# Kernel optimization log

Measured on AMD Instinct MI355X. Metric: run time of the kernel, lower is better.

## Reference

```python
import jax, jax.numpy as jnp
import numpy as np

B, C, L = 32, 512, 4096
H, K = 8, 3            # heads, kernel_size
D = C // H             # head dim
G = 32                 # GroupNorm groups
PAD = (K - 1) // 2
EPS = 1e-5
NEG = -1e30


def setup_inputs() -> dict:
    key = jax.random.key(0)
    ks = jax.random.split(key, 7)
    s = 0.02
    return {
        "x": jax.random.normal(ks[0], (B, C, L), dtype=jnp.float32),
        "gamma": jnp.ones((C,), dtype=jnp.float32),
        "beta": jnp.zeros((C,), dtype=jnp.float32),
        "W_k": jax.random.normal(ks[1], (C, H * D), dtype=jnp.float32) * s,
        "W_v": jax.random.normal(ks[2], (C, H * D), dtype=jnp.float32) * s,
        "W_o": jax.random.normal(ks[3], (H * D, C), dtype=jnp.float32) * s,
        "q": jax.random.normal(ks[4], (H, D), dtype=jnp.float32) * s,     # learned queries (QnA)
        "rpe": jax.random.normal(ks[5], (H, K), dtype=jnp.float32) * s,   # relative-position bias
    }


def _group_norm(x, gamma, beta):
    # x: (B, C, L); normalize over (C//G, L) within each of G groups
    b, c, l = x.shape
    xg = x.reshape(b, G, (c // G) * l)
    mu = jnp.mean(xg, axis=-1, keepdims=True)
    var = jnp.var(xg, axis=-1, keepdims=True)
    xn = ((xg - mu) * jax.lax.rsqrt(var + EPS)).reshape(b, c, l)
    return xn * gamma[None, :, None] + beta[None, :, None]


def reference(x, gamma, beta, W_k, W_v, W_o, q, rpe):
    h = _group_norm(x, gamma, beta)                     # (B, C, L)
    ht = jnp.transpose(h, (0, 2, 1))                    # (B, L, C)
    k = (ht @ W_k).reshape(B, L, H, D)                  # (B, L, H, D)
    v = (ht @ W_v).reshape(B, L, H, D)

    scale = 1.0 / np.sqrt(D).astype(np.float32)
    logits = jnp.einsum('blhd,hd->blh', k, q) * scale   # (B, L, H)

    # sliding windows of size K (zero-padded; -inf logits at boundaries)
    lp = jnp.pad(logits, ((0, 0), (PAD, PAD), (0, 0)), constant_values=NEG)
    lwin = jnp.stack([lp[:, j:j + L] for j in range(K)], axis=2)      # (B, L, K, H)
    lwin = lwin + jnp.transpose(rpe)[None, None]                       # rpe: (H,K)->(K,H)
    attn = jax.nn.softmax(lwin, axis=2)                                # (B, L, K, H)

    vp = jnp.pad(v, ((0, 0), (PAD, PAD), (0, 0), (0, 0)))
    vwin = jnp.stack([vp[:, j:j + L] for j in range(K)], axis=2)       # (B, L, K, H, D)
    o = jnp.einsum('blkh,blkhd->blhd', attn, vwin).reshape(B, L, H * D)

    out = (o @ W_o)                                      # (B, L, C)
    return x + jnp.transpose(out, (0, 2, 1))             # residual, (B, C, L)
```

## Files before the change

kernel.cpp:

```cpp
#include <hip/hip_runtime.h>

#define Bb 32
#define Cc 512
#define Ll 4096
#define Hh 8
#define Dd 64
#define Gg 32
#define BLt (Bb * Ll)
#define NKV 520
#define NKVPAD 640

typedef __attribute__((ext_vector_type(4))) float f32x4;
typedef __attribute__((ext_vector_type(8))) short short8;
typedef __attribute__((ext_vector_type(4))) short s16x4;
typedef __attribute__((ext_vector_type(4))) int int4v;

union U16 { int4v v; short s[8]; };

__device__ __forceinline__ float bf2f(short s) {
    unsigned u = ((unsigned)(unsigned short)s) << 16;
    float f; __builtin_memcpy(&f, &u, 4); return f;
}
__device__ __forceinline__ short f2bf(float f) {
    unsigned u; __builtin_memcpy(&u, &f, 4);
    u = (u + 0x7FFFu + ((u >> 16) & 1u)) >> 16;
    return (short)u;
}

__device__ __forceinline__ int kpack(int k) {
    int blk = k >> 5, r = k & 31;
    return blk * 32 + ((r & 15) >> 2) * 8 + ((r >> 4) << 2) + (r & 3);
}

__device__ __forceinline__ int swz_off(int row, int inner) {
    return row * 128 + (inner ^ ((row & 7) << 4));
}

__device__ __forceinline__ void gload16(const short* g, short* l) {
    __builtin_amdgcn_global_load_lds((const __attribute__((address_space(1))) unsigned int*)g,
                                     (__attribute__((address_space(3))) unsigned int*)l,
                                     16, 0, 0);
}

#define BAR() __builtin_amdgcn_s_barrier()
#define SFENCE() __builtin_amdgcn_sched_barrier(0)

__global__ void k_prep(const float* __restrict__ Wk, const float* __restrict__ Wv,
                       const float* __restrict__ Wo, const float* __restrict__ q,
                       short* __restrict__ Wct, short* __restrict__ Wot, int packWo)
{
    int bid = blockIdx.x, t = threadIdx.x;
    if (bid < NKVPAD) {
        int n = bid;
        if (n < 512) {
            for (int k = t; k < 512; k += 64)
                Wct[n * 512 + kpack(k)] = f2bf(Wv[k * 512 + n]);
        } else if (n < NKV) {
            int h = n - 512;
            for (int k = t; k < 512; k += 64) {
                float acc = 0.f;
                for (int d = 0; d < 64; ++d)
                    acc += Wk[k * 512 + h * 64 + d] * q[h * 64 + d];
                Wct[n * 512 + kpack(k)] = f2bf(acc * 0.125f);
            }
        } else {
            for (int k = t; k < 512; k += 64) Wct[n * 512 + kpack(k)] = 0;
        }
    } else {
        int c = bid - NKVPAD;
        for (int k = t; k < 512; k += 64)
            Wot[c * 512 + (packWo ? kpack(k) : k)] = f2bf(Wo[k * 512 + c]);
    }
}

__global__ void k_stats(const float* __restrict__ x, float* __restrict__ stats)
{
    int bg = blockIdx.x;
    const float* p = x + (size_t)bg * 65536;
    int t = threadIdx.x;
    float s = 0.f, ss = 0.f;
    for (int i = t * 4; i < 65536; i += 1024) {
        f32x4 v = *(const f32x4*)(p + i);
        s  += v[0] + v[1] + v[2] + v[3];
        ss += v[0]*v[0] + v[1]*v[1] + v[2]*v[2] + v[3]*v[3];
    }
    for (int o = 32; o > 0; o >>= 1) { s += __shfl_down(s, o); ss += __shfl_down(ss, o); }
    __shared__ float red[8];
    int lane = t & 63, w = t >> 6;
    if (lane == 0) { red[w] = s; red[4 + w] = ss; }
    __syncthreads();
    if (t == 0) {
        float S  = red[0] + red[1] + red[2] + red[3];
        float SS = red[4] + red[5] + red[6] + red[7];
        float mean = S * (1.0f / 65536.0f);
        float var  = SS * (1.0f / 65536.0f) - mean * mean;
        stats[bg * 2]     = mean;
        stats[bg * 2 + 1] = rsqrtf(var + 1e-5f);
    }
}

__global__ void k_norm_t(const float* __restrict__ x, const float* __restrict__ gamma,
                         const float* __restrict__ beta, const float* __restrict__ stats,
                         short* __restrict__ hT)
{
    __shared__ float tile[64 * 65];
    int b = blockIdx.z, c0 = blockIdx.y * 64, l0 = blockIdx.x * 64;
    int t = threadIdx.x;
    int lq = t & 15, cq = t >> 4;
    #pragma unroll
    for (int p = 0; p < 4; ++p) {
        int cl = cq + p * 16;
        int c = c0 + cl;
        float mean = stats[(b * 32 + (c >> 4)) * 2];
        float rstd = stats[(b * 32 + (c >> 4)) * 2 + 1];
        float a  = rstd * gamma[c];
        float bb = beta[c] - mean * a;
        f32x4 v = *(const f32x4*)(x + ((size_t)b << 21) + ((size_t)c << 12) + l0 + lq * 4);
        #pragma unroll
        for (int j = 0; j < 4; ++j) tile[cl * 65 + lq * 4 + j] = v[j] * a + bb;
    }
    __syncthreads();
    int ll = t >> 2, cq4 = t & 3;
    int bl = b * Ll + l0 + ll;
    short hbuf[16];
    #pragma unroll
    for (int j = 0; j < 16; ++j) hbuf[j] = f2bf(tile[(cq4 * 16 + j) * 65 + ll]);
    short* dst = hT + (size_t)bl * 512 + ((c0 >> 5) + (cq4 >> 1)) * 32 + ((cq4 & 1) << 2);
    #pragma unroll
    for (int jj = 0; jj < 4; ++jj) {
        s16x4 v4 = { hbuf[jj*4+0], hbuf[jj*4+1], hbuf[jj*4+2], hbuf[jj*4+3] };
        *(s16x4*)(dst + jj * 8) = v4;
    }
}


__launch_bounds__(256, 2)
__global__ void k_gemm1f(const short* __restrict__ A, const short* __restrict__ Bw,
                         short* __restrict__ vbuf, short* __restrict__ lbuf)
{
    __shared__ short sA[2][8192];
    __shared__ short sB[2][8192];
    __shared__ short wqlds[8192];
    const int t = threadIdx.x;
    const int nwg = 1024;
    const int bid = blockIdx.x;
    const int work = (bid & 7) * (nwg >> 3) + (bid >> 3);
    const int ntile = work & 3;
    const int n0 = ntile * 128;
    const int mbase = (work >> 2) * 512;

    const int lane = t & 63, wid = t >> 6;
    const int wm = wid >> 1, wn = wid & 1;
    const int g = lane >> 4, ln = lane & 15;

    {
        int row = t >> 5;
        int cp = (t & 31) * 2;
        int4v v0 = *(const int4v*)(Bw + (size_t)(512 + row) * 512 + cp * 8);
        int4v v1 = *(const int4v*)(Bw + (size_t)(512 + row) * 512 + cp * 8 + 8);
        *(int4v*)((char*)wqlds + row * 1024 + ((cp * 16) ^ ((row & 7) << 4))) = v0;
        *(int4v*)((char*)wqlds + row * 1024 + (((cp + 1) * 16) ^ ((row & 7) << 4))) = v1;
        int4v z = {0, 0, 0, 0};
        int row2 = 8 + (t >> 5);
        *(int4v*)((char*)wqlds + row2 * 1024 + ((cp * 16) ^ ((row2 & 7) << 4))) = z;
        *(int4v*)((char*)wqlds + row2 * 1024 + (((cp + 1) * 16) ^ ((row2 & 7) << 4))) = z;
    }
    asm volatile("s_waitcnt vmcnt(0) lgkmcnt(0)" ::: "memory");
    BAR(); SFENCE();

    const int srow = wid * 8 + (lane >> 3);
    const int sinner = (((lane & 7) ^ ((lane >> 3) & 7)) << 3);
    const short* gAs = A  + (size_t)(mbase + srow) * 512 + sinner;
    const short* gBs = Bw + (size_t)(n0 + srow) * 512 + sinner;

    f32x4 acc[4][4] = {};
    f32x4 accq[4] = {};

    auto stage = [&](int kt, int buf) {
        size_t offA = (size_t)(kt >> 3) * 65536 + (size_t)(kt & 7) * 64;
        size_t offB = (size_t)(kt & 7) * 64;
        #pragma unroll
        for (int gq = 0; gq < 4; ++gq) {
            gload16(gAs + (size_t)gq * 32 * 512 + offA, &sA[buf][gq * 2048 + wid * 512]);
            gload16(gBs + (size_t)gq * 32 * 512 + offB, &sB[buf][gq * 2048 + wid * 512]);
        }
    };
    auto compute = [&](int buf, int kk) {
        #pragma unroll
        for (int ks = 0; ks < 2; ++ks) {
            short8 af[4], bfr[4], bq;
            #pragma unroll
            for (int i = 0; i < 4; ++i) {
                af[i]  = *(const short8*)((const char*)&sA[buf][0] + swz_off(wm * 64 + i * 16 + ln, ks * 64 + g * 16));
                bfr[i] = *(const short8*)((const char*)&sB[buf][0] + swz_off(wn * 64 + i * 16 + ln, ks * 64 + g * 16));
            }
            bq = *(const short8*)((const char*)wqlds + ln * 1024 +
                                  ((kk * 128 + ks * 64 + g * 16) ^ ((ln & 7) << 4)));
            #pragma unroll
            for (int mi = 0; mi < 4; ++mi)
                #pragma unroll
                for (int ni = 0; ni < 4; ++ni)
                    acc[mi][ni] = __builtin_amdgcn_mfma_f32_16x16x32_bf16(af[mi], bfr[ni], acc[mi][ni], 0, 0, 0);
            #pragma unroll
            for (int mi = 0; mi < 4; ++mi)
                accq[mi] = __builtin_amdgcn_mfma_f32_16x16x32_bf16(af[mi], bq, accq[mi], 0, 0, 0);
        }
    };

    stage(0, 0); stage(1, 1);
    #pragma unroll 1
    for (int s = 0; s < 32; ++s) {
        if (s == 31)           asm volatile("s_waitcnt vmcnt(0)"  ::: "memory");
        else if ((s & 7) == 0 && s) asm volatile("s_waitcnt vmcnt(16)" ::: "memory");
        else                   asm volatile("s_waitcnt vmcnt(8)"  ::: "memory");
        BAR(); SFENCE();
        compute(s & 1, s & 7);
        SFENCE();
        if ((s & 7) == 7) {
            BAR();
            int m0 = mbase + (s >> 3) * 128;
            {
                short* scrW = &sB[s & 1][0] + wid * 2048;
                const int blkq = (lane & 7) >> 2, jq = lane & 3;
                #pragma unroll
                for (int p = 0; p < 2; ++p) {
                    #pragma unroll
                    for (int mh = 0; mh < 2; ++mh)
                        #pragma unroll
                        for (int ni = 0; ni < 4; ++ni)
                            #pragma unroll
                            for (int i = 0; i < 4; ++i)
                                scrW[(mh * 16 + g * 4 + i) * 64 + ni * 16 + ln] = f2bf(acc[p * 2 + mh][ni][i]);
                    asm volatile("s_waitcnt lgkmcnt(0)" ::: "memory"); SFENCE();
                    #pragma unroll
                    for (int it = 0; it < 4; ++it) {
                        int mrl = it * 8 + (lane >> 3);
                        const short* bp = scrW + mrl * 64 + blkq * 32;
                        s16x4 lo = *(const s16x4*)(bp + 4 * jq);
                        s16x4 hi = *(const s16x4*)(bp + 16 + 4 * jq);
                        union { int4v v; s16x4 h[2]; } ov;
                        ov.h[0] = lo; ov.h[1] = hi;
                        int m = m0 + wm * 64 + p * 32 + mrl;
                        int nc = n0 + wn * 64 + blkq * 32 + jq * 8;
                        *(int4v*)(vbuf + (size_t)m * 512 + nc) = ov.v;
                    }
                    asm volatile("s_waitcnt lgkmcnt(0)" ::: "memory"); SFENCE();
                }
            }
            if (ntile == 0 && wn == 0 && ln < 8) {
                #pragma unroll
                for (int mi = 0; mi < 4; ++mi)
                    #pragma unroll
                    for (int i = 0; i < 4; ++i) {
                        int m = m0 + wm * 64 + mi * 16 + g * 4 + i;
                        lbuf[(size_t)m * 8 + ln] = f2bf(accq[mi][i]);
                    }
            }
            #pragma unroll
            for (int mi = 0; mi < 4; ++mi) {
                #pragma unroll
                for (int ni = 0; ni < 4; ++ni)
                    acc[mi][ni] = (f32x4){0.f, 0.f, 0.f, 0.f};
                accq[mi] = (f32x4){0.f, 0.f, 0.f, 0.f};
            }
        }
        if (s < 30) { BAR(); stage(s + 2, s & 1); SFENCE(); }
    }
}

__global__ void k_combine(const short* __restrict__ vbuf, const short* __restrict__ lbuf,
                          const float* __restrict__ rpe, short* __restrict__ obuf)
{
    int t = threadIdx.x;
    int bl = blockIdx.x * 16 + (t >> 4);
    int blkd = t & 15;
    int h = blkd >> 1;
    int l = bl & (Ll - 1);
    int bm = (l == 0) ? bl : bl - 1;
    int bp = (l == Ll - 1) ? bl : bl + 1;
    float lg0 = (l > 0)      ? bf2f(lbuf[(size_t)bm * 8 + h]) + rpe[h * 3 + 0] : -1e30f;
    float lg1 =                bf2f(lbuf[(size_t)bl * 8 + h]) + rpe[h * 3 + 1];
    float lg2 = (l < Ll - 1) ? bf2f(lbuf[(size_t)bp * 8 + h]) + rpe[h * 3 + 2] : -1e30f;
    float m = fmaxf(lg1, fmaxf(lg0, lg2));
    float e0 = (l > 0)      ? __expf(lg0 - m) : 0.f;
    float e1 =                __expf(lg1 - m);
    float e2 = (l < Ll - 1) ? __expf(lg2 - m) : 0.f;
    float inv = 1.0f / (e0 + e1 + e2);
    float w0 = e0 * inv, w1 = e1 * inv, w2 = e2 * inv;

    const short8* vm = (const short8*)(vbuf + (size_t)bm * 512 + blkd * 32);
    const short8* v0 = (const short8*)(vbuf + (size_t)bl * 512 + blkd * 32);
    const short8* vp = (const short8*)(vbuf + (size_t)bp * 512 + blkd * 32);
    short8* dst = (short8*)(obuf + (size_t)bl * 512 + blkd * 32);
    #pragma unroll
    for (int qq = 0; qq < 4; ++qq) {
        short8 a = vm[qq], b = v0[qq], c = vp[qq], r;
        #pragma unroll
        for (int j = 0; j < 8; ++j)
            r[j] = f2bf(w0 * bf2f(a[j]) + w1 * bf2f(b[j]) + w2 * bf2f(c[j]));
        dst[qq] = r;
    }
}

__launch_bounds__(256, 2)
__global__ void k_gemm2f(const short* __restrict__ Wot, const short* __restrict__ obuf,
                         const float* __restrict__ x, float* __restrict__ out)
{
    __shared__ short sA[2][8192];
    __shared__ short sB[3][8192];
    const int t = threadIdx.x;
    const int nwg = 1024;
    const int bid = blockIdx.x;
    const int work = (bid & 7) * (nwg >> 3) + (bid >> 3);
    const int n0 = work * 128;

    const int lane = t & 63, wid = t >> 6;
    const int wm = wid >> 1, wn = wid & 1;
    const int g = lane >> 4, ln = lane & 15;

    const int srow = wid * 8 + (lane >> 3);
    const int sinner = (((lane & 7) ^ ((lane >> 3) & 7)) << 3);
    const short* gAs = Wot  + (size_t)srow * 512 + sinner;
    const short* gBs = obuf + (size_t)(n0 + srow) * 512 + sinner;

    const int r4 = lane >> 4, lcm = (lane & 15) * 4;
    const int ngE = n0 + wn * 64 + lcm;
    const size_t rowbase = ((size_t)(ngE >> 12) << 21) + (size_t)(ngE & (Ll - 1));
    const float* xrow = x + rowbase;
    float* outrow = out + rowbase;

    f32x4 acc[4][4] = {};
    f32x4 xp[4][4];

    auto stageA = [&](int s, int buf) {
        size_t off = (size_t)(s >> 3) * 65536 + (size_t)(s & 7) * 64;
        #pragma unroll
        for (int gq = 0; gq < 4; ++gq)
            gload16(gAs + (size_t)gq * 32 * 512 + off, &sA[buf][gq * 2048 + wid * 512]);
    };
    auto stageB = [&](int s, int buf) {
        size_t off = (size_t)(s & 7) * 64;
        #pragma unroll
        for (int gq = 0; gq < 4; ++gq)
            gload16(gBs + (size_t)gq * 32 * 512 + off, &sB[buf][gq * 2048 + wid * 512]);
    };
    auto xpf = [&](int tile) {
        int cb = tile * 128 + wm * 64;
        #pragma unroll
        for (int p = 0; p < 4; ++p)
            #pragma unroll
            for (int j = 0; j < 4; ++j)
                xp[p][j] = *(const f32x4*)(xrow + ((size_t)(cb + p * 16 + r4 + 4 * j) << 12));
    };
    auto compute = [&](int ab, int bb) {
        #pragma unroll
        for (int ks = 0; ks < 2; ++ks) {
            short8 af[4], bfr[4];
            #pragma unroll
            for (int i = 0; i < 4; ++i) {
                af[i]  = *(const short8*)((const char*)&sA[ab][0] + swz_off(wm * 64 + i * 16 + ln, ks * 64 + g * 16));
                bfr[i] = *(const short8*)((const char*)&sB[bb][0] + swz_off(wn * 64 + i * 16 + ln, ks * 64 + g * 16));
            }
            #pragma unroll
            for (int mi = 0; mi < 4; ++mi)
                #pragma unroll
                for (int ni = 0; ni < 4; ++ni)
                    acc[mi][ni] = __builtin_amdgcn_mfma_f32_16x16x32_bf16(af[mi], bfr[ni], acc[mi][ni], 0, 0, 0);
        }
    };

    stageA(0, 0); stageA(1, 1); stageB(0, 0); stageB(1, 1); stageB(2, 2);
    #pragma unroll 1
    for (int s = 0; s < 32; ++s) {
        if (s == 0)             asm volatile("s_waitcnt vmcnt(8)"  ::: "memory");
        else if (s == 31)       asm volatile("s_waitcnt vmcnt(0)"  ::: "memory");
        else if (s == 30)       asm volatile("s_waitcnt vmcnt(8)"  ::: "memory");
        else if ((s & 7) <= 2)  asm volatile("s_waitcnt vmcnt(28)" ::: "memory");
        else                    asm volatile("s_waitcnt vmcnt(12)" ::: "memory");
        BAR(); SFENCE();
        compute(s & 1, s % 3);
        SFENCE();
        if ((s & 7) == 7) {
            BAR();
            float* scr = (float*)((char*)&sA[s & 1][0] + wid * 4096);
            int m0c = (s >> 3) * 128;
            #pragma unroll
            for (int p = 0; p < 4; ++p) {
                #pragma unroll
                for (int ni = 0; ni < 4; ++ni)
                    #pragma unroll
                    for (int i = 0; i < 4; ++i) {
                        int r = g * 4 + i;
                        int col = (ni * 16 + ln) ^ ((((r & 3) ^ (r >> 2)) & 3) << 4);
                        scr[r * 64 + col] = acc[p][ni][i];
                    }
                asm volatile("s_waitcnt lgkmcnt(0)" ::: "memory"); SFENCE();
                #pragma unroll
                for (int j = 0; j < 4; ++j) {
                    int rr = r4 + 4 * j;
                    int cst = lcm ^ ((((rr & 3) ^ (rr >> 2)) & 3) << 4);
                    f32x4 sv = *(const f32x4*)&scr[rr * 64 + cst];
                    int c = m0c + wm * 64 + p * 16 + rr;
                    *(f32x4*)(outrow + ((size_t)c << 12)) = xp[p][j] + sv;
                }
                asm volatile("s_waitcnt lgkmcnt(0)" ::: "memory"); SFENCE();
            }
            #pragma unroll
            for (int mi = 0; mi < 4; ++mi)
                #pragma unroll
                for (int ni = 0; ni < 4; ++ni)
                    acc[mi][ni] = (f32x4){0.f, 0.f, 0.f, 0.f};
        }
        if (s < 30) {
            BAR();
            stageA(s + 2, s & 1);
            if (s < 29) stageB(s + 3, (s + 3) % 3);
            if ((s & 7) == 0) xpf(s >> 3);
            SFENCE();
        }
    }
}

__launch_bounds__(256, 2)
__global__ void k_gemm1_fb(const short* __restrict__ A, const short* __restrict__ Bw,
                           short* __restrict__ kv)
{
    __shared__ short sA[2][8192];
    __shared__ short sB[2][8192];
    const int t = threadIdx.x;
    const int m0 = blockIdx.y * 128;
    const int n0 = blockIdx.x * 128;
    const int lane = t & 63, wid = t >> 6;
    const int wm = wid >> 1, wn = wid & 1;
    const int g = lane >> 4, ln = lane & 15;

    const int srow = wid * 8 + (lane >> 3);
    const int sinner = (((lane & 7) ^ ((lane >> 3) & 7)) << 3);
    const short* gAs = A  + (size_t)(m0 + srow) * 512 + sinner;
    const short* gBs = Bw + (size_t)(n0 + srow) * 512 + sinner;

    f32x4 acc[4][4] = {};

    auto stage = [&](int kt, int buf) {
        #pragma unroll
        for (int gq = 0; gq < 4; ++gq) {
            gload16(gAs + (size_t)gq * 32 * 512 + kt * 64, &sA[buf][gq * 2048 + wid * 512]);
            gload16(gBs + (size_t)gq * 32 * 512 + kt * 64, &sB[buf][gq * 2048 + wid * 512]);
        }
    };
    auto compute = [&](int buf) {
        #pragma unroll
        for (int ks = 0; ks < 2; ++ks) {
            short8 af[4], bfr[4];
            #pragma unroll
            for (int i = 0; i < 4; ++i) {
                af[i]  = *(const short8*)((const char*)&sA[buf][0] + swz_off(wm * 64 + i * 16 + ln, ks * 64 + g * 16));
                bfr[i] = *(const short8*)((const char*)&sB[buf][0] + swz_off(wn * 64 + i * 16 + ln, ks * 64 + g * 16));
            }
            #pragma unroll
            for (int mi = 0; mi < 4; ++mi)
                #pragma unroll
                for (int ni = 0; ni < 4; ++ni)
                    acc[mi][ni] = __builtin_amdgcn_mfma_f32_16x16x32_bf16(af[mi], bfr[ni], acc[mi][ni], 0, 0, 0);
        }
    };

    stage(0, 0);
    __syncthreads();
    #pragma unroll 1
    for (int kt = 0; kt < 8; ++kt) {
        if (kt < 7) stage(kt + 1, (kt + 1) & 1);
        compute(kt & 1);
        __syncthreads();
    }

    #pragma unroll
    for (int mi = 0; mi < 4; ++mi)
        #pragma unroll
        for (int ni = 0; ni < 4; ++ni) {
            int n = n0 + wn * 64 + ni * 16 + ln;
            if (n < NKV) {
                #pragma unroll
                for (int i = 0; i < 4; ++i) {
                    int m = m0 + wm * 64 + mi * 16 + g * 4 + i;
                    kv[(size_t)m * NKV + n] = f2bf(acc[mi][ni][i]);
                }
            }
        }
}

__global__ void k_attnw(const short* __restrict__ kv, const float* __restrict__ rpe,
                        float* __restrict__ attnW)
{
    int tid = blockIdx.x * 256 + threadIdx.x;
    int bl = tid >> 3, h = tid & 7;
    int l = bl & (Ll - 1);
    float lg[3];
    #pragma unroll
    for (int j = 0; j < 3; ++j) {
        bool valid = (j == 1) || (j == 0 && l > 0) || (j == 2 && l < Ll - 1);
        lg[j] = valid ? (bf2f(kv[(size_t)(bl + j - 1) * NKV + 512 + h]) + rpe[h * 3 + j])
                      : -1e30f;
    }
    float m = fmaxf(lg[0], fmaxf(lg[1], lg[2]));
    float e0 = __expf(lg[0] - m), e1 = __expf(lg[1] - m), e2 = __expf(lg[2] - m);
    float inv = 1.0f / (e0 + e1 + e2);
    f32x4 w = { e0 * inv, e1 * inv, e2 * inv, 0.0f };
    *(f32x4*)(attnW + (size_t)bl * 32 + h * 4) = w;
}

__launch_bounds__(256, 2)
__global__ void k_gemm2_fused(const short* __restrict__ Wot, const short* __restrict__ kv,
                              const float* __restrict__ attnW, const float* __restrict__ x,
                              float* __restrict__ out)
{
    __shared__ short sA[2][8192];
    __shared__ short sB[2][8192];
    const int t = threadIdx.x;
    const int m0 = blockIdx.x * 128;
    const int n0 = blockIdx.y * 128;
    const int lane = t & 63, wid = t >> 6;
    const int wm = wid >> 1, wn = wid & 1;
    const int g = lane >> 4, ln = lane & 15;
    const int sr = t >> 1, ksh = t & 1;

    const short* gA = Wot + (size_t)(m0 + sr) * 512 + ksh * 32;
    const int nrow = n0 + sr;
    const int lpos = nrow & (Ll - 1);
    const int nm1 = (lpos == 0) ? nrow : nrow - 1;
    const int np1 = (lpos == Ll - 1) ? nrow : nrow + 1;
    const short* gV0 = kv + (size_t)nrow * NKV + ksh * 32;
    const short* gVm = kv + (size_t)nm1  * NKV + ksh * 32;
    const short* gVp = kv + (size_t)np1  * NKV + ksh * 32;
    const float* gW = attnW + (size_t)nrow * 32;

    f32x4 acc[4][4] = {};
    U16 ra[4], rbm[4], rb0[4], rbp[4];
    f32x4 wv;

    auto load_tile = [&](int kt) {
        #pragma unroll
        for (int qq = 0; qq < 4; ++qq) {
            ra[qq].v  = *(const int4v*)(gA  + kt * 64 + qq * 8);
            rbm[qq].v = *(const int4v*)(gVm + kt * 64 + qq * 8);
            rb0[qq].v = *(const int4v*)(gV0 + kt * 64 + qq * 8);
            rbp[qq].v = *(const int4v*)(gVp + kt * 64 + qq * 8);
        }
        wv = *(const f32x4*)(gW + kt * 4);
    };
    auto write_tile = [&](int buf) {
        short ob[32];
        #pragma unroll
        for (int qq = 0; qq < 4; ++qq)
            #pragma unroll
            for (int j = 0; j < 8; ++j) {
                float o = wv[0] * bf2f(rbm[qq].s[j]) + wv[1] * bf2f(rb0[qq].s[j])
                        + wv[2] * bf2f(rbp[qq].s[j]);
                ob[qq * 8 + j] = f2bf(o);
            }
        #pragma unroll
        for (int f = 0; f < 4; ++f) {
            U16 wa, wb;
            #pragma unroll
            for (int j = 0; j < 4; ++j) {
                wa.s[j]     = ra[f >> 1].s[(f & 1) * 4 + j];
                wa.s[4 + j] = ra[2 + (f >> 1)].s[(f & 1) * 4 + j];
                wb.s[j]     = ob[4 * f + j];
                wb.s[4 + j] = ob[16 + 4 * f + j];
            }
            int off = swz_off(sr, ksh * 64 + f * 16);
            *(int4v*)((char*)&sA[buf][0] + off) = wa.v;
            *(int4v*)((char*)&sB[buf][0] + off) = wb.v;
        }
    };
    auto compute = [&](int buf) {
        #pragma unroll
        for (int ks = 0; ks < 2; ++ks) {
            short8 af[4], bfr[4];
            #pragma unroll
            for (int i = 0; i < 4; ++i) {
                af[i]  = *(const short8*)((const char*)&sA[buf][0] + swz_off(wm * 64 + i * 16 + ln, ks * 64 + g * 16));
                bfr[i] = *(const short8*)((const char*)&sB[buf][0] + swz_off(wn * 64 + i * 16 + ln, ks * 64 + g * 16));
            }
            #pragma unroll
            for (int mi = 0; mi < 4; ++mi)
                #pragma unroll
                for (int ni = 0; ni < 4; ++ni)
                    acc[mi][ni] = __builtin_amdgcn_mfma_f32_16x16x32_bf16(af[mi], bfr[ni], acc[mi][ni], 0, 0, 0);
        }
    };

    load_tile(0); write_tile(0); __syncthreads();
    #pragma unroll 1
    for (int kt = 0; kt < 8; ++kt) {
        if (kt < 7) load_tile(kt + 1);
        compute(kt & 1);
        if (kt < 7) write_tile((kt + 1) & 1);
        __syncthreads();
    }

    #pragma unroll
    for (int mi = 0; mi < 4; ++mi)
        #pragma unroll
        for (int ni = 0; ni < 4; ++ni)
            #pragma unroll
            for (int i = 0; i < 4; ++i) {
                int c = m0 + wm * 64 + mi * 16 + g * 4 + i;
                int ng = n0 + wn * 64 + ni * 16 + ln;
                int b = ng >> 12, l = ng & (Ll - 1);
                size_t off = ((size_t)b << 21) | ((size_t)c << 12) | (size_t)l;
                out[off] = x[off] + acc[mi][ni][i];
            }
}

extern "C" void kernel_launch(void* const* d_in, const int* in_sizes, int n_in,
                              void* d_out, int out_size, void* d_ws, size_t ws_size,
                              hipStream_t stream)
{
    const float* x     = (const float*)d_in[0];
    const float* gamma = (const float*)d_in[1];
    const float* beta  = (const float*)d_in[2];
    const float* Wk    = (const float*)d_in[3];
    const float* Wv    = (const float*)d_in[4];
    const float* Wo    = (const float*)d_in[5];
    const float* q     = (const float*)d_in[6];
    const float* rpe   = (const float*)d_in[7];
    float* out = (float*)d_out;
    char* ws = (char*)d_ws;

    const size_t MB128 = 134217728ull;
    const size_t MAIN_WS = MB128 * 2 + 655360 + 524288 + 2097152 + 8192;

    if (ws_size >= MAIN_WS) {
        short* obuf  = (short*)(ws);
        short* vbuf  = (short*)(ws + MB128);
        short* Wct   = (short*)(ws + 2 * MB128);
        short* Wot   = (short*)(ws + 2 * MB128 + 655360);
        short* lbuf  = (short*)(ws + 2 * MB128 + 655360 + 524288);
        float* stats = (float*)(ws + 2 * MB128 + 655360 + 524288 + 2097152);
        short* hT    = (short*)d_out;

        k_prep<<<1152, 64, 0, stream>>>(Wk, Wv, Wo, q, Wct, Wot, 1);
        k_stats<<<1024, 256, 0, stream>>>(x, stats);
        k_norm_t<<<dim3(64, 8, 32), 256, 0, stream>>>(x, gamma, beta, stats, hT);
        k_gemm1f<<<1024, 256, 0, stream>>>(hT, Wct, vbuf, lbuf);
        k_combine<<<8192, 256, 0, stream>>>(vbuf, lbuf, rpe, obuf);
        k_gemm2f<<<1024, 256, 0, stream>>>(Wot, obuf, x, out);
    } else {
        short* Wct   = (short*)(ws + 0);
        short* Wot   = (short*)(ws + 655360);
        float* stats = (float*)(ws + 1179648);
        float* attnW = (float*)(ws + 1187840);
        short* kv    = (short*)(ws + 17965056);
        short* hT    = (short*)d_out;

        k_prep<<<1152, 64, 0, stream>>>(Wk, Wv, Wo, q, Wct, Wot, 0);
        k_stats<<<1024, 256, 0, stream>>>(x, stats);
        k_norm_t<<<dim3(64, 8, 32), 256, 0, stream>>>(x, gamma, beta, stats, hT);
        k_gemm1_fb<<<dim3(5, 1024), 256, 0, stream>>>(hT, Wct, kv);
        k_attnw<<<4096, 256, 0, stream>>>(kv, rpe, attnW);
        k_gemm2_fused<<<dim3(4, 1024), 256, 0, stream>>>(Wot, kv, attnW, x, out);
    }
}
```

Baseline: 545.6 us.

## Fuse windowed attention combine into output GEMM B-operand staging

Replaces the separate combine kernel, which wrote a full bf16 obuf, with a small kernel that writes only per-position softmax weights. The output GEMM now loads the three neighbouring V rows into registers, mixes them with the weights from LDS, and writes the combined bf16 tile into LDS as its B operand. This removes one full write and re-read of a 128 MB intermediate. In exchange, V reads in the GEMM triple, the pipeline becomes synchronous with vmcnt(0) waits every step, and the x prefetch becomes an inline load in the epilogue.

```diff
diff --git a/kernel.cpp b/kernel.cpp
--- a/kernel.cpp
+++ b/kernel.cpp
@@ -37,6 +37,11 @@
 }
 
 __device__ __forceinline__ void gload16(const short* g, short* l) {
+    __builtin_amdgcn_global_load_lds((const __attribute__((address_space(1))) unsigned int*)g,
+                                     (__attribute__((address_space(3))) unsigned int*)l,
+                                     16, 0, 0);
+}
+__device__ __forceinline__ void gload16f(const float* g, float* l) {
     __builtin_amdgcn_global_load_lds((const __attribute__((address_space(1))) unsigned int*)g,
                                      (__attribute__((address_space(3))) unsigned int*)l,
                                      16, 0, 0);
@@ -132,7 +137,6 @@
         *(s16x4*)(dst + jj * 8) = v4;
     }
 }
-
 
 __launch_bounds__(256, 2)
 __global__ void k_gemm1f(const short* __restrict__ A, const short* __restrict__ Bw,
@@ -268,46 +272,32 @@
     }
 }
 
-__global__ void k_combine(const short* __restrict__ vbuf, const short* __restrict__ lbuf,
-                          const float* __restrict__ rpe, short* __restrict__ obuf)
-{
-    int t = threadIdx.x;
-    int bl = blockIdx.x * 16 + (t >> 4);
-    int blkd = t & 15;
-    int h = blkd >> 1;
+__global__ void k_attnw2(const short* __restrict__ lbuf, const float* __restrict__ rpe,
+                         float* __restrict__ attnW)
+{
+    int tid = blockIdx.x * 256 + threadIdx.x;
+    int bl = tid >> 3, h = tid & 7;
     int l = bl & (Ll - 1);
-    int bm = (l == 0) ? bl : bl - 1;
-    int bp = (l == Ll - 1) ? bl : bl + 1;
-    float lg0 = (l > 0)      ? bf2f(lbuf[(size_t)bm * 8 + h]) + rpe[h * 3 + 0] : -1e30f;
-    float lg1 =                bf2f(lbuf[(size_t)bl * 8 + h]) + rpe[h * 3 + 1];
-    float lg2 = (l < Ll - 1) ? bf2f(lbuf[(size_t)bp * 8 + h]) + rpe[h * 3 + 2] : -1e30f;
+    float lg0 = (l > 0)      ? bf2f(lbuf[(size_t)(bl - 1) * 8 + h]) + rpe[h * 3 + 0] : -1e30f;
+    float lg1 =                bf2f(lbuf[(size_t)bl * 8 + h])       + rpe[h * 3 + 1];
+    float lg2 = (l < Ll - 1) ? bf2f(lbuf[(size_t)(bl + 1) * 8 + h]) + rpe[h * 3 + 2] : -1e30f;
     float m = fmaxf(lg1, fmaxf(lg0, lg2));
     float e0 = (l > 0)      ? __expf(lg0 - m) : 0.f;
     float e1 =                __expf(lg1 - m);
     float e2 = (l < Ll - 1) ? __expf(lg2 - m) : 0.f;
     float inv = 1.0f / (e0 + e1 + e2);
-    float w0 = e0 * inv, w1 = e1 * inv, w2 = e2 * inv;
-
-    const short8* vm = (const short8*)(vbuf + (size_t)bm * 512 + blkd * 32);
-    const short8* v0 = (const short8*)(vbuf + (size_t)bl * 512 + blkd * 32);
-    const short8* vp = (const short8*)(vbuf + (size_t)bp * 512 + blkd * 32);
-    short8* dst = (short8*)(obuf + (size_t)bl * 512 + blkd * 32);
-    #pragma unroll
-    for (int qq = 0; qq < 4; ++qq) {
-        short8 a = vm[qq], b = v0[qq], c = vp[qq], r;
-        #pragma unroll
-        for (int j = 0; j < 8; ++j)
-            r[j] = f2bf(w0 * bf2f(a[j]) + w1 * bf2f(b[j]) + w2 * bf2f(c[j]));
-        dst[qq] = r;
-    }
+    f32x4 w = { e0 * inv, e1 * inv, e2 * inv, 0.0f };
+    *(f32x4*)(attnW + (size_t)bl * 32 + h * 4) = w;
 }
 
 __launch_bounds__(256, 2)
-__global__ void k_gemm2f(const short* __restrict__ Wot, const short* __restrict__ obuf,
-                         const float* __restrict__ x, float* __restrict__ out)
+__global__ void k_gemm2f(const short* __restrict__ Wot, const short* __restrict__ vbuf,
+                         const float* __restrict__ attnW, const float* __restrict__ x,
+                         float* __restrict__ out)
 {
     __shared__ short sA[2][8192];
-    __shared__ short sB[3][8192];
+    __shared__ short sBc[2][8192];
+    __shared__ float wlds[4096];
     const int t = threadIdx.x;
     const int nwg = 1024;
     const int bid = blockIdx.x;
@@ -320,8 +310,19 @@
 
     const int srow = wid * 8 + (lane >> 3);
     const int sinner = (((lane & 7) ^ ((lane >> 3) & 7)) << 3);
-    const short* gAs = Wot  + (size_t)srow * 512 + sinner;
-    const short* gBs = obuf + (size_t)(n0 + srow) * 512 + sinner;
+    const short* gAs = Wot + (size_t)srow * 512 + sinner;
+
+    const short* gV0[4]; const short* gVm[4]; const short* gVp[4];
+    #pragma unroll
+    for (int q2 = 0; q2 < 4; ++q2) {
+        int r = n0 + srow + 32 * q2;
+        int l = r & (Ll - 1);
+        int rm = (l == 0) ? r : r - 1;
+        int rp = (l == Ll - 1) ? r : r + 1;
+        gV0[q2] = vbuf + (size_t)r  * 512 + sinner;
+        gVm[q2] = vbuf + (size_t)rm * 512 + sinner;
+        gVp[q2] = vbuf + (size_t)rp * 512 + sinner;
+    }
 
     const int r4 = lane >> 4, lcm = (lane & 15) * 4;
     const int ngE = n0 + wn * 64 + lcm;
@@ -330,7 +331,7 @@
     float* outrow = out + rowbase;
 
     f32x4 acc[4][4] = {};
-    f32x4 xp[4][4];
+    U16 Rm[4], R0[4], Rp[4];
 
     auto stageA = [&](int s, int buf) {
         size_t off = (size_t)(s >> 3) * 65536 + (size_t)(s & 7) * 64;
@@ -338,28 +339,39 @@
         for (int gq = 0; gq < 4; ++gq)
             gload16(gAs + (size_t)gq * 32 * 512 + off, &sA[buf][gq * 2048 + wid * 512]);
     };
-    auto stageB = [&](int s, int buf) {
-        size_t off = (size_t)(s & 7) * 64;
-        #pragma unroll
-        for (int gq = 0; gq < 4; ++gq)
-            gload16(gBs + (size_t)gq * 32 * 512 + off, &sB[buf][gq * 2048 + wid * 512]);
-    };
-    auto xpf = [&](int tile) {
-        int cb = tile * 128 + wm * 64;
-        #pragma unroll
-        for (int p = 0; p < 4; ++p)
-            #pragma unroll
-            for (int j = 0; j < 4; ++j)
-                xp[p][j] = *(const f32x4*)(xrow + ((size_t)(cb + p * 16 + r4 + 4 * j) << 12));
-    };
-    auto compute = [&](int ab, int bb) {
+    auto loadR = [&](int s1) {
+        size_t off = (size_t)(s1 & 7) * 64;
+        #pragma unroll
+        for (int q2 = 0; q2 < 4; ++q2) {
+            Rm[q2].v = *(const int4v*)(gVm[q2] + off);
+            R0[q2].v = *(const int4v*)(gV0[q2] + off);
+            Rp[q2].v = *(const int4v*)(gVp[q2] + off);
+        }
+    };
+    auto combineStep = [&](int s1, int buf) {
+        int h = s1 & 7;
+        #pragma unroll
+        for (int q2 = 0; q2 < 4; ++q2) {
+            int r = srow + 32 * q2;
+            f32x4 w = *(const f32x4*)&wlds[r * 32 + ((h ^ (r & 7)) << 2)];
+            U16 cm;
+            #pragma unroll
+            for (int j = 0; j < 8; ++j) {
+                float o = w[0] * bf2f(Rm[q2].s[j]) + w[1] * bf2f(R0[q2].s[j])
+                        + w[2] * bf2f(Rp[q2].s[j]);
+                cm.s[j] = f2bf(o);
+            }
+            *(int4v*)((char*)&sBc[buf][0] + q2 * 4096 + wid * 1024 + lane * 16) = cm.v;
+        }
+    };
+    auto compute = [&](int buf) {
         #pragma unroll
         for (int ks = 0; ks < 2; ++ks) {
             short8 af[4], bfr[4];
             #pragma unroll
             for (int i = 0; i < 4; ++i) {
-                af[i]  = *(const short8*)((const char*)&sA[ab][0] + swz_off(wm * 64 + i * 16 + ln, ks * 64 + g * 16));
-                bfr[i] = *(const short8*)((const char*)&sB[bb][0] + swz_off(wn * 64 + i * 16 + ln, ks * 64 + g * 16));
+                af[i]  = *(const short8*)((const char*)&sA[buf][0] + swz_off(wm * 64 + i * 16 + ln, ks * 64 + g * 16));
+                bfr[i] = *(const short8*)((const char*)&sBc[buf][0] + swz_off(wn * 64 + i * 16 + ln, ks * 64 + g * 16));
             }
             #pragma unroll
             for (int mi = 0; mi < 4; ++mi)
@@ -369,17 +381,30 @@
         }
     };
 
-    stageA(0, 0); stageA(1, 1); stageB(0, 0); stageB(1, 1); stageB(2, 2);
+    stageA(0, 0); stageA(1, 1);
+    {
+        const float* wsrc = attnW + (size_t)n0 * 32;
+        int rr = lane >> 3, hl = lane & 7;
+        #pragma unroll
+        for (int j = 0; j < 4; ++j) {
+            int row = (wid * 4 + j) * 8 + rr;
+            gload16f(wsrc + row * 32 + ((hl ^ (row & 7)) << 2), &wlds[(wid * 4 + j) * 256]);
+        }
+    }
+    loadR(0); SFENCE();
+    asm volatile("s_waitcnt vmcnt(0)" ::: "memory");
+    BAR(); SFENCE();
+    combineStep(0, 0);
+    asm volatile("s_waitcnt lgkmcnt(0)" ::: "memory");
+    loadR(1); SFENCE();
+
     #pragma unroll 1
     for (int s = 0; s < 32; ++s) {
-        if (s == 0)             asm volatile("s_waitcnt vmcnt(8)"  ::: "memory");
-        else if (s == 31)       asm volatile("s_waitcnt vmcnt(0)"  ::: "memory");
-        else if (s == 30)       asm volatile("s_waitcnt vmcnt(8)"  ::: "memory");
-        else if ((s & 7) <= 2)  asm volatile("s_waitcnt vmcnt(28)" ::: "memory");
-        else                    asm volatile("s_waitcnt vmcnt(12)" ::: "memory");
+        asm volatile("s_waitcnt vmcnt(0)" ::: "memory");
         BAR(); SFENCE();
-        compute(s & 1, s % 3);
-        SFENCE();
+        if (s < 31) combineStep(s + 1, (s + 1) & 1);
+        compute(s & 1);
+        asm volatile("s_waitcnt lgkmcnt(0)" ::: "memory"); SFENCE();
         if ((s & 7) == 7) {
             BAR();
             float* scr = (float*)((char*)&sA[s & 1][0] + wid * 4096);
@@ -401,7 +426,8 @@
                     int cst = lcm ^ ((((rr & 3) ^ (rr >> 2)) & 3) << 4);
                     f32x4 sv = *(const f32x4*)&scr[rr * 64 + cst];
                     int c = m0c + wm * 64 + p * 16 + rr;
-                    *(f32x4*)(outrow + ((size_t)c << 12)) = xp[p][j] + sv;
+                    f32x4 xv = *(const f32x4*)(xrow + ((size_t)c << 12));
+                    *(f32x4*)(outrow + ((size_t)c << 12)) = xv + sv;
                 }
                 asm volatile("s_waitcnt lgkmcnt(0)" ::: "memory"); SFENCE();
             }
@@ -414,8 +440,7 @@
         if (s < 30) {
             BAR();
             stageA(s + 2, s & 1);
-            if (s < 29) stageB(s + 3, (s + 3) % 3);
-            if ((s & 7) == 0) xpf(s >> 3);
+            loadR(s + 2);
             SFENCE();
         }
     }
@@ -632,7 +657,7 @@
     const size_t MAIN_WS = MB128 * 2 + 655360 + 524288 + 2097152 + 8192;
 
     if (ws_size >= MAIN_WS) {
-        short* obuf  = (short*)(ws);
+        float* attnW = (float*)(ws);
         short* vbuf  = (short*)(ws + MB128);
         short* Wct   = (short*)(ws + 2 * MB128);
         short* Wot   = (short*)(ws + 2 * MB128 + 655360);
@@ -644,8 +669,8 @@
         k_stats<<<1024, 256, 0, stream>>>(x, stats);
         k_norm_t<<<dim3(64, 8, 32), 256, 0, stream>>>(x, gamma, beta, stats, hT);
         k_gemm1f<<<1024, 256, 0, stream>>>(hT, Wct, vbuf, lbuf);
-        k_combine<<<8192, 256, 0, stream>>>(vbuf, lbuf, rpe, obuf);
-        k_gemm2f<<<1024, 256, 0, stream>>>(Wot, obuf, x, out);
+        k_attnw2<<<4096, 256, 0, stream>>>(lbuf, rpe, attnW);
+        k_gemm2f<<<1024, 256, 0, stream>>>(Wot, vbuf, attnW, x, out);
     } else {
         short* Wct   = (short*)(ws + 0);
         short* Wot   = (short*)(ws + 655360);
```

After: 522.7 us. 4.2% less time.
